# Kernel optimization log

Measured on AMD Instinct MI355X. Metric: run time of the kernel, lower is better.

Reference implementation:

```python
import jax, jax.numpy as jnp
import numpy as np
import math

PC_MIN_X, PC_MIN_Y = 0.0, -40.0
VOXEL = 0.05
STRIDE = 8
PE_CH = 16
NEG_SLOPE = 0.01
BN_EPS = 1e-5


def _grid_points():
    # get_pseudo_points: centers of stride-8 BEV cells
    xs = np.arange(0.2, 70.4, 0.4, dtype=np.float32)    # 176
    ys = np.arange(-39.8, 40.2, 0.4, dtype=np.float32)  # 200
    gx, gy = np.meshgrid(xs, ys)                        # (200, 176)
    return jnp.asarray(np.stack([gx, gy], -1).reshape(-1, 2))  # [P, 2]


def _pe3d(D, H, W):
    ch = PE_CH
    div = jnp.exp(jnp.arange(0, ch, 2, dtype=jnp.float32) * (-math.log(10000.0) / ch))
    def enc(n):
        t = jnp.arange(n, dtype=jnp.float32)[:, None] * div[None, :]
        return jnp.concatenate([jnp.sin(t), jnp.cos(t)], axis=-1)  # [n, ch]
    pex = jnp.broadcast_to(enc(D)[:, None, None, :], (D, H, W, ch))
    pey = jnp.broadcast_to(enc(H)[None, :, None, :], (D, H, W, ch))
    pez = jnp.broadcast_to(enc(W)[None, None, :, :], (D, H, W, ch))
    return jnp.concatenate([pex, pey, pez], axis=-1).transpose(3, 0, 1, 2)  # [3*ch, D, H, W]


def _bn_lrelu(h, g, b):
    # eval-mode BatchNorm3d with running_mean=0, running_var=1, then LeakyReLU(0.01)
    h = h * (g / np.sqrt(1.0 + BN_EPS))[None, :, None, None, None] + b[None, :, None, None, None]
    return jnp.where(h >= 0, h, NEG_SLOPE * h)


def _dvf(x, w1, b1, g1, be1, w2, b2, g2, be2, w3, b3):
    N, C, D, H, W = x.shape
    pe = _pe3d(D, H, W)  # [48, D, H, W]
    feats = jnp.concatenate([x, jnp.broadcast_to(pe[None], (N,) + pe.shape)], axis=1)
    h = jnp.einsum('ncdhw,oc->nodhw', feats, w1) + b1[None, :, None, None, None]
    h = _bn_lrelu(h, g1, be1)
    h = jnp.einsum('ncdhw,oc->nodhw', h, w2) + b2[None, :, None, None, None]
    h = _bn_lrelu(h, g2, be2)
    logits = jnp.einsum('ncdhw,oc->nodhw', h, w3) + b3[None, :, None, None, None]  # [N,1,D,H,W]
    wts = jax.nn.softmax(logits, axis=2)  # softmax over depth D
    return (x * wts).reshape(N, C * D, H, W)


def _bilinear(im, x, y):
    # im: (H, W, C), x/y: (P,)  -- faithful to bilinear_interpolate_torch
    H, W = im.shape[0], im.shape[1]
    xf = jnp.floor(x).astype(jnp.int32)
    yf = jnp.floor(y).astype(jnp.int32)
    x0 = jnp.clip(xf, 0, W - 1)
    x1 = jnp.clip(xf + 1, 0, W - 1)
    y0 = jnp.clip(yf, 0, H - 1)
    y1 = jnp.clip(yf + 1, 0, H - 1)
    Ia, Ib, Ic, Id = im[y0, x0], im[y1, x0], im[y0, x1], im[y1, x1]
    x0f, x1f = x0.astype(x.dtype), x1.astype(x.dtype)
    y0f, y1f = y0.astype(y.dtype), y1.astype(y.dtype)
    wa = (x1f - x) * (y1f - y)
    wb = (x1f - x) * (y - y0f)
    wc = (x - x0f) * (y1f - y)
    wd = (x - x0f) * (y - y0f)
    return Ia * wa[:, None] + Ib * wb[:, None] + Ic * wc[:, None] + Id * wd[:, None]


def _rot(p, theta):
    c, s = jnp.cos(theta), jnp.sin(theta)
    return jnp.stack([p[:, 0] * c - p[:, 1] * s, p[:, 0] * s + p[:, 1] * c], axis=-1)


def _bev_align_one(feat, th_prev, th_cur, grid):
    # feat: [C', H, W]; X_TRANS modeled as z-rotation: fwd(current) then inverse(previous)
    Hh, Ww = feat.shape[1], feat.shape[2]
    p = _rot(grid, th_cur)
    p = _rot(p, -th_prev)
    xi = (p[:, 0] - PC_MIN_X) / VOXEL / STRIDE
    yi = (p[:, 1] - PC_MIN_Y) / VOXEL / STRIDE
    out = _bilinear(feat.transpose(1, 2, 0), xi, yi)  # [P, C']
    return out.reshape(Hh, Ww, -1).transpose(2, 0, 1)


def setup_inputs() -> dict:
    key = jax.random.key(0)
    ks = jax.random.split(key, 16)
    N, C, D, H, W = 4, 64, 2, 200, 176
    IN1 = PE_CH * 3 + C  # 112
    inp = {
        'x0': jax.random.normal(ks[0], (N, C, D, H, W), jnp.float32),
        'x1': jax.random.normal(ks[1], (N, C, D, H, W), jnp.float32),
        'transform_param': jax.random.normal(ks[2], (N, 2), jnp.float32) * 0.3,
        'w1': jax.random.normal(ks[3], (C, IN1), jnp.float32) * 0.05,
        'b1': jax.random.normal(ks[4], (C,), jnp.float32) * 0.05,
        'g1': jax.random.uniform(ks[5], (C,), jnp.float32, 0.5, 1.5),
        'be1': jax.random.normal(ks[6], (C,), jnp.float32) * 0.05,
        'w2': jax.random.normal(ks[7], (C // 2, C), jnp.float32) * 0.05,
        'b2': jax.random.normal(ks[8], (C // 2,), jnp.float32) * 0.05,
        'g2': jax.random.uniform(ks[9], (C // 2,), jnp.float32, 0.5, 1.5),
        'be2': jax.random.normal(ks[10], (C // 2,), jnp.float32) * 0.05,
        'w3': jax.random.normal(ks[11], (1, C // 2), jnp.float32) * 0.05,
        'b3': jax.random.normal(ks[12], (1,), jnp.float32) * 0.05,
    }
    return inp


def reference(x0, x1, transform_param, w1, b1, g1, be1, w2, b2, g2, be2, w3, b3):
    mlp = (w1, b1, g1, be1, w2, b2, g2, be2, w3, b3)
    f0 = _dvf(x0, *mlp)  # rot 0: [N, C*D, H, W]
    f1 = _dvf(x1, *mlp)  # rot 1
    grid = _grid_points()
    aligned = jax.vmap(lambda f, tp: _bev_align_one(f, tp[0], tp[1], grid))(f1, transform_param)
    return jnp.maximum(f0, aligned)  # ALIGN_METHOD='max' over stacked feats
```

## Files before the change

kernel.cpp:

```cpp
#include <hip/hip_runtime.h>
#include <cmath>

#define HW   35200
#define CD   128

typedef short bf16x8 __attribute__((ext_vector_type(8)));
typedef float f32x4  __attribute__((ext_vector_type(4)));

#define OFF_W1B   0
#define OFF_W2B   3072
#define OFF_TD    4096
#define OFF_B2F   4224
#define OFF_W3F   4256
#define OFF_PE    4288
#define OFF_F0B   567488
#define OFF_F1B   9578688

__device__ __forceinline__ float lrelu(float v) { return v >= 0.f ? v : 0.01f * v; }
__device__ __forceinline__ unsigned short f2bf(float f) {
  unsigned u = __float_as_uint(f);
  u = (u + 0x7fffu + ((u >> 16) & 1u)) >> 16;
  return (unsigned short)u;
}
__device__ __forceinline__ float bflo(unsigned u) { return __uint_as_float(u << 16); }
__device__ __forceinline__ float bfhi(unsigned u) { return __uint_as_float(u & 0xffff0000u); }

__global__ void setup_kernel(const float* __restrict__ w1, const float* __restrict__ b1,
                             const float* __restrict__ g1, const float* __restrict__ be1,
                             const float* __restrict__ w2, const float* __restrict__ b2,
                             const float* __restrict__ g2, const float* __restrict__ be2,
                             const float* __restrict__ w3, const float* __restrict__ b3,
                             float* __restrict__ ws) {
  const float RS = rsqrtf(1.0f + 1e-5f);
  unsigned short* w1b = (unsigned short*)(ws + OFF_W1B);
  unsigned short* w2b = (unsigned short*)(ws + OFF_W2B);
  unsigned short* pe  = (unsigned short*)(ws + OFF_PE);
  int i = blockIdx.x * blockDim.x + threadIdx.x;
  if (i < 6144) {
    int e = i & 7, l = (i >> 3) & 63, nt = (i >> 9) & 3, kh = i >> 11;
    int n = nt * 16 + (l & 15);
    int k = kh * 32 + (l >> 4) * 8 + e;
    int col = (kh < 2) ? k : (80 + (k - 64));
    w1b[i] = f2bf(w1[n * 112 + col] * (g1[n] * RS));
    return;
  }
  i -= 6144;
  if (i < 2048) {
    int e = i & 7, l = (i >> 3) & 63, nt = (i >> 9) & 1, kh = i >> 10;
    int n = nt * 16 + (l & 15);
    int k = kh * 32 + (l >> 4) * 8 + e;
    w2b[i] = f2bf(w2[n * 64 + k] * (g2[n] * RS));
    return;
  }
  i -= 2048;
  if (i < 128) {
    int d = i >> 6, o = i & 63;
    float a = 0.f;
    for (int j = 0; j < 8; ++j) {
      float dv = expf((float)(2 * j) * (-0.5756462732485115f));
      float t  = (float)d * dv;
      a += w1[o * 112 + 64 + j] * sinf(t) + w1[o * 112 + 72 + j] * cosf(t);
    }
    ws[OFF_TD + d * 64 + o] = (g1[o] * RS) * (b1[o] + a) + be1[o];
    return;
  }
  i -= 128;
  if (i < 32) { ws[OFF_B2F + i] = b2[i] * (g2[i] * RS) + be2[i]; return; }
  i -= 32;
  if (i < 32) { ws[OFF_W3F + i] = w3[i]; return; }
  i -= 32;
  if (i < 563200) {
    int hw = i >> 4, j = i & 15;
    int h = hw / 176, w = hw - h * 176;
    int jj = j & 7;
    float dv = expf((float)(2 * jj) * (-0.5756462732485115f));
    if (j < 8) {
      float t = (float)h * dv;
      pe[hw * 32 + jj]      = f2bf(sinf(t));
      pe[hw * 32 + 8 + jj]  = f2bf(cosf(t));
    } else {
      float t = (float)w * dv;
      pe[hw * 32 + 16 + jj] = f2bf(sinf(t));
      pe[hw * 32 + 24 + jj] = f2bf(cosf(t));
    }
  }
}

__global__ __launch_bounds__(256, 4)
void mlp_kernel(const float* __restrict__ x0, const float* __restrict__ x1,
                const float* __restrict__ wtab,
                unsigned short* __restrict__ f0b, unsigned short* __restrict__ f1b) {
  __shared__ alignas(16) unsigned short As[12 * 128 * 8];
  unsigned short* Hs = As;
  float* lgp  = (float*)(As + 8 * 128 * 8);
  float* wtsp = lgp + 128;

  const int t    = threadIdx.x;
  const int lane = t & 63;
  const int wv   = __builtin_amdgcn_readfirstlane(t >> 6);
  const int px   = lane;
  const int n    = blockIdx.y;
  const int inp  = blockIdx.z;
  const int hw0  = blockIdx.x * 64;
  const float* xn = (inp ? x1 : x0) + (size_t)n * CD * HW;
  unsigned short* dst = inp ? f1b : f0b;
  const unsigned short* w1bu = (const unsigned short*)(wtab + OFF_W1B);
  const unsigned short* w2bu = (const unsigned short*)(wtab + OFF_W2B);
  const unsigned short* peg  = (const unsigned short*)(wtab + OFF_PE);

  unsigned xr[4][4];
#pragma unroll
  for (int i2 = 0; i2 < 4; ++i2) {
    const int md = wv * 4 + i2, d = md & 1, m = md >> 1;
    float v[8];
#pragma unroll
    for (int e = 0; e < 8; ++e)
      v[e] = xn[(size_t)((m * 8 + e) * 2 + d) * HW + hw0 + px];
    uint4 uu;
    uu.x = (unsigned)f2bf(v[0]) | ((unsigned)f2bf(v[1]) << 16);
    uu.y = (unsigned)f2bf(v[2]) | ((unsigned)f2bf(v[3]) << 16);
    uu.z = (unsigned)f2bf(v[4]) | ((unsigned)f2bf(v[5]) << 16);
    uu.w = (unsigned)f2bf(v[6]) | ((unsigned)f2bf(v[7]) << 16);
    xr[i2][0] = uu.x; xr[i2][1] = uu.y; xr[i2][2] = uu.z; xr[i2][3] = uu.w;
    *(uint4*)&As[(unsigned)(m * 128 + d * 64 + px) * 8] = uu;
  }
  {
    const uint4 v = *(const uint4*)(peg + (size_t)(hw0 + px) * 32 + wv * 8);
    *(uint4*)&As[(unsigned)((8 + wv) * 128 + px) * 8]      = v;
    *(uint4*)&As[(unsigned)((8 + wv) * 128 + 64 + px) * 8] = v;
  }
  __syncthreads();

  const int rtb = wv * 2, dw = wv >> 1;
  f32x4 acc[2][4];
#pragma unroll
  for (int nt = 0; nt < 4; ++nt) {
    const float tdv = wtab[OFF_TD + dw * 64 + nt * 16 + (lane & 15)];
    acc[0][nt] = (f32x4){tdv, tdv, tdv, tdv};
    acc[1][nt] = acc[0][nt];
  }
#pragma unroll
  for (int kh = 0; kh < 3; ++kh) {
    const bf16x8 a0 = *(const bf16x8*)&As[(unsigned)((kh * 4 + (lane >> 4)) * 128 + (rtb + 0) * 16 + (lane & 15)) * 8];
    const bf16x8 a1 = *(const bf16x8*)&As[(unsigned)((kh * 4 + (lane >> 4)) * 128 + (rtb + 1) * 16 + (lane & 15)) * 8];
#pragma unroll
    for (int nt = 0; nt < 4; ++nt) {
      const bf16x8 b = *(const bf16x8*)&w1bu[(unsigned)((kh * 4 + nt) * 64 + lane) * 8];
      acc[0][nt] = __builtin_amdgcn_mfma_f32_16x16x32_bf16(a0, b, acc[0][nt], 0, 0, 0);
      acc[1][nt] = __builtin_amdgcn_mfma_f32_16x16x32_bf16(a1, b, acc[1][nt], 0, 0, 0);
    }
  }
  __syncthreads();

#pragma unroll
  for (int rti = 0; rti < 2; ++rti)
#pragma unroll
    for (int nt = 0; nt < 4; ++nt)
#pragma unroll
      for (int r = 0; r < 4; ++r) {
        const int o   = nt * 16 + (lane & 15);
        const int row = (rtb + rti) * 16 + (lane >> 4) * 4 + r;
        Hs[(unsigned)((o >> 3) * 128 + row) * 8 + (o & 7)] = f2bf(lrelu(acc[rti][nt][r]));
      }
  __syncthreads();

  f32x4 acc2[2][2];
#pragma unroll
  for (int nt = 0; nt < 2; ++nt) {
    const float bv = wtab[OFF_B2F + nt * 16 + (lane & 15)];
    acc2[0][nt] = (f32x4){bv, bv, bv, bv};
    acc2[1][nt] = acc2[0][nt];
  }
#pragma unroll
  for (int kh = 0; kh < 2; ++kh) {
    const bf16x8 a0 = *(const bf16x8*)&Hs[(unsigned)((kh * 4 + (lane >> 4)) * 128 + (rtb + 0) * 16 + (lane & 15)) * 8];
    const bf16x8 a1 = *(const bf16x8*)&Hs[(unsigned)((kh * 4 + (lane >> 4)) * 128 + (rtb + 1) * 16 + (lane & 15)) * 8];
#pragma unroll
    for (int nt = 0; nt < 2; ++nt) {
      const bf16x8 b = *(const bf16x8*)&w2bu[(unsigned)((kh * 2 + nt) * 64 + lane) * 8];
      acc2[0][nt] = __builtin_amdgcn_mfma_f32_16x16x32_bf16(a0, b, acc2[0][nt], 0, 0, 0);
      acc2[1][nt] = __builtin_amdgcn_mfma_f32_16x16x32_bf16(a1, b, acc2[1][nt], 0, 0, 0);
    }
  }

  const float w3a = wtab[OFF_W3F + (lane & 15)];
  const float w3b = wtab[OFF_W3F + 16 + (lane & 15)];
#pragma unroll
  for (int rti = 0; rti < 2; ++rti)
#pragma unroll
    for (int r = 0; r < 4; ++r) {
      float p = w3a * lrelu(acc2[rti][0][r]) + w3b * lrelu(acc2[rti][1][r]);
      p += __shfl_xor(p, 1);
      p += __shfl_xor(p, 2);
      p += __shfl_xor(p, 4);
      p += __shfl_xor(p, 8);
      if ((lane & 15) == 0) lgp[(rtb + rti) * 16 + (lane >> 4) * 4 + r] = p;
    }
  __syncthreads();

  if (t < 128) {
    const int pp = t & 63, dd = t >> 6;
    const float lm = lgp[dd * 64 + pp], lo = lgp[(1 - dd) * 64 + pp];
    wtsp[dd * 64 + pp] = 1.f / (1.f + expf(lo - lm));
  }
  __syncthreads();

  const float w0 = wtsp[px], w1v = wtsp[64 + px];
#pragma unroll
  for (int i2 = 0; i2 < 8; ++i2) {
    const int k = wv * 8 + i2;
    const unsigned ua = xr[2 * (i2 >> 2) + 0][i2 & 3];
    const unsigned ub = xr[2 * (i2 >> 2) + 1][i2 & 3];
    const unsigned short v0 = f2bf(bflo(ua) * w0);
    const unsigned short v1 = f2bf(bflo(ub) * w1v);
    const unsigned short v2 = f2bf(bfhi(ua) * w0);
    const unsigned short v3 = f2bf(bfhi(ub) * w1v);
    uint2 pk;
    pk.x = (unsigned)v0 | ((unsigned)v1 << 16);
    pk.y = (unsigned)v2 | ((unsigned)v3 << 16);
    *(uint2*)&dst[(((size_t)n * 32 + k) * HW + hw0 + px) * 4] = pk;
  }
}

__global__ __launch_bounds__(256)
void gather_max_kernel(const unsigned short* __restrict__ f0b,
                       const unsigned short* __restrict__ f1b,
                       const float* __restrict__ tp,
                       float* __restrict__ out) {
  const int orig = blockIdx.x;
  const int xcd = orig & 7, idx = orig >> 3;
  const int tile = (xcd < 6 ? xcd * 69 : 6 * 69 + (xcd - 6) * 68) + idx;

  const int tix = threadIdx.x;
  const int px  = tix & 63;
  const int q   = tix >> 6;
  const int n   = blockIdx.y;
  const int hw  = tile * 64 + px;
  const int h   = hw / 176;
  const int w   = hw - h * 176;

  const float thp = tp[n * 2 + 0], thc = tp[n * 2 + 1];
  const float gx = 0.2f + 0.4f * (float)w;
  const float gy = -39.8f + 0.4f * (float)h;
  const float c1 = cosf(thc),  s1v = sinf(thc);
  const float p1x = gx * c1 - gy * s1v;
  const float p1y = gx * s1v + gy * c1;
  const float c2 = cosf(-thp), s2v = sinf(-thp);
  const float p2x = p1x * c2 - p1y * s2v;
  const float p2y = p1x * s2v + p1y * c2;
  const float xi = p2x / 0.05f / 8.f;
  const float yi = (p2y - (-40.f)) / 0.05f / 8.f;

  const float xf = floorf(xi), yf = floorf(yi);
  const int x0i = (int)xf, y0i = (int)yf;
  const int x0c = min(max(x0i,     0), 175);
  const int x1c = min(max(x0i + 1, 0), 175);
  const int y0c = min(max(y0i,     0), 199);
  const int y1c = min(max(y0i + 1, 0), 199);
  const float x0f = (float)x0c, x1f = (float)x1c;
  const float y0f = (float)y0c, y1f = (float)y1c;
  const float wa = (x1f - xi) * (y1f - yi);
  const float wb = (x1f - xi) * (yi - y0f);
  const float wc = (xi - x0f) * (y1f - yi);
  const float wd = (xi - x0f) * (yi - y0f);
  const int ta = y0c * 176 + x0c, tb = y1c * 176 + x0c;
  const int tc = y0c * 176 + x1c, td = y1c * 176 + x1c;

#pragma unroll
  for (int i = 0; i < 8; ++i) {
    const int k = q * 8 + i;
    const int cd0 = k * 4;
    const unsigned short* fp1 = f1b + ((size_t)n * 32 + k) * HW * 4;
    const uint2 Ia = *(const uint2*)(fp1 + (size_t)ta * 4);
    const uint2 Ib = *(const uint2*)(fp1 + (size_t)tb * 4);
    const uint2 Ic = *(const uint2*)(fp1 + (size_t)tc * 4);
    const uint2 Id = *(const uint2*)(fp1 + (size_t)td * 4);
    float4 sv;
    sv.x = bflo(Ia.x) * wa + bflo(Ib.x) * wb + bflo(Ic.x) * wc + bflo(Id.x) * wd;
    sv.y = bfhi(Ia.x) * wa + bfhi(Ib.x) * wb + bfhi(Ic.x) * wc + bfhi(Id.x) * wd;
    sv.z = bflo(Ia.y) * wa + bflo(Ib.y) * wb + bflo(Ic.y) * wc + bflo(Id.y) * wd;
    sv.w = bfhi(Ia.y) * wa + bfhi(Ib.y) * wb + bfhi(Ic.y) * wc + bfhi(Id.y) * wd;

    const uint2 F0 = *(const uint2*)(f0b + (((size_t)n * 32 + k) * HW + hw) * 4);

    float* op = out + ((size_t)n * CD + cd0) * HW + hw;
    op[0]              = fmaxf(bflo(F0.x), sv.x);
    op[HW]             = fmaxf(bfhi(F0.x), sv.y);
    op[2 * (size_t)HW] = fmaxf(bflo(F0.y), sv.z);
    op[3 * (size_t)HW] = fmaxf(bfhi(F0.y), sv.w);
  }
}

extern "C" void kernel_launch(void* const* d_in, const int* in_sizes, int n_in,
                              void* d_out, int out_size, void* d_ws, size_t ws_size,
                              hipStream_t stream) {
  const float* x0  = (const float*)d_in[0];
  const float* x1  = (const float*)d_in[1];
  const float* tp  = (const float*)d_in[2];
  const float* w1  = (const float*)d_in[3];
  const float* b1  = (const float*)d_in[4];
  const float* g1  = (const float*)d_in[5];
  const float* be1 = (const float*)d_in[6];
  const float* w2  = (const float*)d_in[7];
  const float* b2  = (const float*)d_in[8];
  const float* g2  = (const float*)d_in[9];
  const float* be2 = (const float*)d_in[10];
  const float* w3  = (const float*)d_in[11];
  const float* b3  = (const float*)d_in[12];
  float* ws = (float*)d_ws;
  unsigned short* f0b = (unsigned short*)(ws + OFF_F0B);
  unsigned short* f1b = (unsigned short*)(ws + OFF_F1B);

  setup_kernel<<<2233, 256, 0, stream>>>(w1, b1, g1, be1, w2, b2, g2, be2, w3, b3, ws);

  dim3 g1d(550, 4, 2);
  mlp_kernel<<<g1d, 256, 0, stream>>>(x0, x1, ws, f0b, f1b);

  dim3 g2d(550, 4);
  gather_max_kernel<<<g2d, 256, 0, stream>>>(f0b, f1b, tp, (float*)d_out);
}
```

Before: 93.66 us.

## Load MLP input fragments directly into MFMA registers, skipping LDS staging

The first MLP layer now builds its MFMA A-operands straight from global loads in each wave's registers, in the fragment layout the instruction expects, instead of staging inputs and positional encodings through shared memory. Each wave now owns 16 pixels for both depth slices. Because the depth softmax can then be computed inside the wave from shuffled logits, two barriers and the shared logits buffer go away. The cost is that global loads are less coalesced: each lane reads 16 pixel-contiguous values per channel group instead of 64, which may increase memory transactions.

```diff
diff --git a/kernel.cpp b/kernel.cpp
--- a/kernel.cpp
+++ b/kernel.cpp
@@ -6,6 +6,8 @@
 
 typedef short bf16x8 __attribute__((ext_vector_type(8)));
 typedef float f32x4  __attribute__((ext_vector_type(4)));
+
+union Frag { unsigned u[4]; bf16x8 v; };
 
 #define OFF_W1B   0
 #define OFF_W2B   3072
@@ -90,91 +92,95 @@
 void mlp_kernel(const float* __restrict__ x0, const float* __restrict__ x1,
                 const float* __restrict__ wtab,
                 unsigned short* __restrict__ f0b, unsigned short* __restrict__ f1b) {
-  __shared__ alignas(16) unsigned short As[12 * 128 * 8];
-  unsigned short* Hs = As;
-  float* lgp  = (float*)(As + 8 * 128 * 8);
-  float* wtsp = lgp + 128;
+  __shared__ alignas(16) unsigned short Hs[8 * 128 * 8];
+  __shared__ float wts[2][64];
 
   const int t    = threadIdx.x;
   const int lane = t & 63;
   const int wv   = __builtin_amdgcn_readfirstlane(t >> 6);
-  const int px   = lane;
+  const int g    = lane >> 4;
+  const int li   = lane & 15;
   const int n    = blockIdx.y;
   const int inp  = blockIdx.z;
   const int hw0  = blockIdx.x * 64;
+  const int pxs  = wv * 16 + li;
   const float* xn = (inp ? x1 : x0) + (size_t)n * CD * HW;
   unsigned short* dst = inp ? f1b : f0b;
   const unsigned short* w1bu = (const unsigned short*)(wtab + OFF_W1B);
   const unsigned short* w2bu = (const unsigned short*)(wtab + OFF_W2B);
   const unsigned short* peg  = (const unsigned short*)(wtab + OFF_PE);
 
-  unsigned xr[4][4];
-#pragma unroll
-  for (int i2 = 0; i2 < 4; ++i2) {
-    const int md = wv * 4 + i2, d = md & 1, m = md >> 1;
-    float v[8];
-#pragma unroll
-    for (int e = 0; e < 8; ++e)
-      v[e] = xn[(size_t)((m * 8 + e) * 2 + d) * HW + hw0 + px];
-    uint4 uu;
-    uu.x = (unsigned)f2bf(v[0]) | ((unsigned)f2bf(v[1]) << 16);
-    uu.y = (unsigned)f2bf(v[2]) | ((unsigned)f2bf(v[3]) << 16);
-    uu.z = (unsigned)f2bf(v[4]) | ((unsigned)f2bf(v[5]) << 16);
-    uu.w = (unsigned)f2bf(v[6]) | ((unsigned)f2bf(v[7]) << 16);
-    xr[i2][0] = uu.x; xr[i2][1] = uu.y; xr[i2][2] = uu.z; xr[i2][3] = uu.w;
-    *(uint4*)&As[(unsigned)(m * 128 + d * 64 + px) * 8] = uu;
-  }
-  {
-    const uint4 v = *(const uint4*)(peg + (size_t)(hw0 + px) * 32 + wv * 8);
-    *(uint4*)&As[(unsigned)((8 + wv) * 128 + px) * 8]      = v;
-    *(uint4*)&As[(unsigned)((8 + wv) * 128 + 64 + px) * 8] = v;
-  }
-  __syncthreads();
-
-  const int rtb = wv * 2, dw = wv >> 1;
+  float xf[2][2][8];
+#pragma unroll
+  for (int ti = 0; ti < 2; ++ti)
+#pragma unroll
+    for (int kh = 0; kh < 2; ++kh)
+#pragma unroll
+      for (int e = 0; e < 8; ++e) {
+        const int c = kh * 32 + g * 8 + e;
+        xf[ti][kh][e] = xn[(size_t)(c * 2 + ti) * HW + hw0 + pxs];
+      }
+  const uint4 pev = *(const uint4*)(peg + (size_t)(hw0 + pxs) * 32 + g * 8);
+
+  Frag xb[2][2];
+#pragma unroll
+  for (int ti = 0; ti < 2; ++ti)
+#pragma unroll
+    for (int kh = 0; kh < 2; ++kh)
+#pragma unroll
+      for (int q = 0; q < 4; ++q)
+        xb[ti][kh].u[q] = (unsigned)f2bf(xf[ti][kh][2 * q])
+                        | ((unsigned)f2bf(xf[ti][kh][2 * q + 1]) << 16);
+  Frag pf;
+  pf.u[0] = pev.x; pf.u[1] = pev.y; pf.u[2] = pev.z; pf.u[3] = pev.w;
+
   f32x4 acc[2][4];
 #pragma unroll
-  for (int nt = 0; nt < 4; ++nt) {
-    const float tdv = wtab[OFF_TD + dw * 64 + nt * 16 + (lane & 15)];
-    acc[0][nt] = (f32x4){tdv, tdv, tdv, tdv};
-    acc[1][nt] = acc[0][nt];
-  }
-#pragma unroll
-  for (int kh = 0; kh < 3; ++kh) {
-    const bf16x8 a0 = *(const bf16x8*)&As[(unsigned)((kh * 4 + (lane >> 4)) * 128 + (rtb + 0) * 16 + (lane & 15)) * 8];
-    const bf16x8 a1 = *(const bf16x8*)&As[(unsigned)((kh * 4 + (lane >> 4)) * 128 + (rtb + 1) * 16 + (lane & 15)) * 8];
+  for (int ti = 0; ti < 2; ++ti)
+#pragma unroll
+    for (int nt = 0; nt < 4; ++nt) {
+      const float tdv = wtab[OFF_TD + ti * 64 + nt * 16 + li];
+      acc[ti][nt] = (f32x4){tdv, tdv, tdv, tdv};
+    }
+#pragma unroll
+  for (int kh = 0; kh < 2; ++kh)
 #pragma unroll
     for (int nt = 0; nt < 4; ++nt) {
       const bf16x8 b = *(const bf16x8*)&w1bu[(unsigned)((kh * 4 + nt) * 64 + lane) * 8];
-      acc[0][nt] = __builtin_amdgcn_mfma_f32_16x16x32_bf16(a0, b, acc[0][nt], 0, 0, 0);
-      acc[1][nt] = __builtin_amdgcn_mfma_f32_16x16x32_bf16(a1, b, acc[1][nt], 0, 0, 0);
-    }
-  }
-  __syncthreads();
-
-#pragma unroll
-  for (int rti = 0; rti < 2; ++rti)
+      acc[0][nt] = __builtin_amdgcn_mfma_f32_16x16x32_bf16(xb[0][kh].v, b, acc[0][nt], 0, 0, 0);
+      acc[1][nt] = __builtin_amdgcn_mfma_f32_16x16x32_bf16(xb[1][kh].v, b, acc[1][nt], 0, 0, 0);
+    }
+#pragma unroll
+  for (int nt = 0; nt < 4; ++nt) {
+    const bf16x8 b = *(const bf16x8*)&w1bu[(unsigned)((8 + nt) * 64 + lane) * 8];
+    acc[0][nt] = __builtin_amdgcn_mfma_f32_16x16x32_bf16(pf.v, b, acc[0][nt], 0, 0, 0);
+    acc[1][nt] = __builtin_amdgcn_mfma_f32_16x16x32_bf16(pf.v, b, acc[1][nt], 0, 0, 0);
+  }
+
+#pragma unroll
+  for (int ti = 0; ti < 2; ++ti) {
+    const int tau = wv + ti * 4;
 #pragma unroll
     for (int nt = 0; nt < 4; ++nt)
 #pragma unroll
       for (int r = 0; r < 4; ++r) {
-        const int o   = nt * 16 + (lane & 15);
-        const int row = (rtb + rti) * 16 + (lane >> 4) * 4 + r;
-        Hs[(unsigned)((o >> 3) * 128 + row) * 8 + (o & 7)] = f2bf(lrelu(acc[rti][nt][r]));
+        const int o   = nt * 16 + li;
+        const int row = tau * 16 + g * 4 + r;
+        Hs[(unsigned)((o >> 3) * 128 + row) * 8 + (o & 7)] = f2bf(lrelu(acc[ti][nt][r]));
       }
-  __syncthreads();
+  }
 
   f32x4 acc2[2][2];
 #pragma unroll
   for (int nt = 0; nt < 2; ++nt) {
-    const float bv = wtab[OFF_B2F + nt * 16 + (lane & 15)];
+    const float bv = wtab[OFF_B2F + nt * 16 + li];
     acc2[0][nt] = (f32x4){bv, bv, bv, bv};
     acc2[1][nt] = acc2[0][nt];
   }
 #pragma unroll
   for (int kh = 0; kh < 2; ++kh) {
-    const bf16x8 a0 = *(const bf16x8*)&Hs[(unsigned)((kh * 4 + (lane >> 4)) * 128 + (rtb + 0) * 16 + (lane & 15)) * 8];
-    const bf16x8 a1 = *(const bf16x8*)&Hs[(unsigned)((kh * 4 + (lane >> 4)) * 128 + (rtb + 1) * 16 + (lane & 15)) * 8];
+    const bf16x8 a0 = *(const bf16x8*)&Hs[(unsigned)((kh * 4 + g) * 128 + (wv + 0) * 16 + li) * 8];
+    const bf16x8 a1 = *(const bf16x8*)&Hs[(unsigned)((kh * 4 + g) * 128 + (wv + 4) * 16 + li) * 8];
 #pragma unroll
     for (int nt = 0; nt < 2; ++nt) {
       const bf16x8 b = *(const bf16x8*)&w2bu[(unsigned)((kh * 2 + nt) * 64 + lane) * 8];
@@ -183,43 +189,43 @@
     }
   }
 
-  const float w3a = wtab[OFF_W3F + (lane & 15)];
-  const float w3b = wtab[OFF_W3F + 16 + (lane & 15)];
-#pragma unroll
-  for (int rti = 0; rti < 2; ++rti)
+  const float w3a = wtab[OFF_W3F + li];
+  const float w3b = wtab[OFF_W3F + 16 + li];
+  float wt0[4], wt1[4];
+#pragma unroll
+  for (int r = 0; r < 4; ++r) {
+    float p0 = w3a * lrelu(acc2[0][0][r]) + w3b * lrelu(acc2[0][1][r]);
+    float p1 = w3a * lrelu(acc2[1][0][r]) + w3b * lrelu(acc2[1][1][r]);
+    p0 += __shfl_xor(p0, 1); p0 += __shfl_xor(p0, 2);
+    p0 += __shfl_xor(p0, 4); p0 += __shfl_xor(p0, 8);
+    p1 += __shfl_xor(p1, 1); p1 += __shfl_xor(p1, 2);
+    p1 += __shfl_xor(p1, 4); p1 += __shfl_xor(p1, 8);
+    wt0[r] = 1.f / (1.f + expf(p1 - p0));
+    wt1[r] = 1.f / (1.f + expf(p0 - p1));
+  }
+  if (li == 0) {
 #pragma unroll
     for (int r = 0; r < 4; ++r) {
-      float p = w3a * lrelu(acc2[rti][0][r]) + w3b * lrelu(acc2[rti][1][r]);
-      p += __shfl_xor(p, 1);
-      p += __shfl_xor(p, 2);
-      p += __shfl_xor(p, 4);
-      p += __shfl_xor(p, 8);
-      if ((lane & 15) == 0) lgp[(rtb + rti) * 16 + (lane >> 4) * 4 + r] = p;
-    }
+      wts[0][wv * 16 + g * 4 + r] = wt0[r];
+      wts[1][wv * 16 + g * 4 + r] = wt1[r];
+    }
+  }
   __syncthreads();
 
-  if (t < 128) {
-    const int pp = t & 63, dd = t >> 6;
-    const float lm = lgp[dd * 64 + pp], lo = lgp[(1 - dd) * 64 + pp];
-    wtsp[dd * 64 + pp] = 1.f / (1.f + expf(lo - lm));
-  }
-  __syncthreads();
-
-  const float w0 = wtsp[px], w1v = wtsp[64 + px];
-#pragma unroll
-  for (int i2 = 0; i2 < 8; ++i2) {
-    const int k = wv * 8 + i2;
-    const unsigned ua = xr[2 * (i2 >> 2) + 0][i2 & 3];
-    const unsigned ub = xr[2 * (i2 >> 2) + 1][i2 & 3];
-    const unsigned short v0 = f2bf(bflo(ua) * w0);
-    const unsigned short v1 = f2bf(bflo(ub) * w1v);
-    const unsigned short v2 = f2bf(bfhi(ua) * w0);
-    const unsigned short v3 = f2bf(bfhi(ub) * w1v);
-    uint2 pk;
-    pk.x = (unsigned)v0 | ((unsigned)v1 << 16);
-    pk.y = (unsigned)v2 | ((unsigned)v3 << 16);
-    *(uint2*)&dst[(((size_t)n * 32 + k) * HW + hw0 + px) * 4] = pk;
-  }
+  const float w0  = wts[0][pxs];
+  const float w1v = wts[1][pxs];
+#pragma unroll
+  for (int kh = 0; kh < 2; ++kh)
+#pragma unroll
+    for (int j = 0; j < 4; ++j) {
+      const int k = kh * 16 + g * 4 + j;
+      const unsigned ua = xb[0][kh].u[j];
+      const unsigned ub = xb[1][kh].u[j];
+      uint2 pk;
+      pk.x = (unsigned)f2bf(bflo(ua) * w0) | ((unsigned)f2bf(bflo(ub) * w1v) << 16);
+      pk.y = (unsigned)f2bf(bfhi(ua) * w0) | ((unsigned)f2bf(bfhi(ub) * w1v) << 16);
+      *(uint2*)&dst[(((size_t)n * 32 + k) * HW + hw0 + pxs) * 4] = pk;
+    }
 }
 
 __global__ __launch_bounds__(256)
```

Result: faster. 90.62 us (-3.2%).
